# Kernel tuning notes

Hardware: AMD Instinct MI355X
Metric: run time of the kernel (lower is better)

The kernel has to match this reference:

```python
import jax, jax.numpy as jnp
import numpy as np

NUM_HEADS = 12


def get_rel_pos(q_size, k_size, rel_pos):
    # rel_pos: (2*max(q,k)-1, head_dim); sizes match table here so no resize.
    max_rel_dist = int(2 * max(q_size, k_size) - 1)
    if rel_pos.shape[0] != max_rel_dist:
        rel_pos = jax.image.resize(rel_pos, (max_rel_dist, rel_pos.shape[1]), method='linear')
    q_coords = jnp.arange(q_size)[:, None] * max(k_size / q_size, 1.0)
    k_coords = jnp.arange(k_size)[None, :] * max(q_size / k_size, 1.0)
    rel = (q_coords - k_coords + (k_size - 1) * max(q_size / k_size, 1.0)).astype(jnp.int32)
    return rel_pos[rel.reshape(-1)].reshape(q_size, k_size, -1)  # (q, k, head_dim)


def setup_inputs() -> dict:
    key = jax.random.key(0)
    ks = jax.random.split(key, 7)
    B, H, W, C = 8, 32, 32, 768
    head_dim = C // NUM_HEADS
    return {
        'x': jax.random.normal(ks[0], (B, H, W, C), jnp.float32),
        'w_qkv': jax.random.normal(ks[1], (C, 3 * C), jnp.float32) * 0.02,
        'b_qkv': jnp.zeros((3 * C,), jnp.float32),
        'rel_pos_h': jax.random.normal(ks[2], (2 * H - 1, head_dim), jnp.float32) * 0.02,
        'rel_pos_w': jax.random.normal(ks[3], (2 * W - 1, head_dim), jnp.float32) * 0.02,
        'w_proj': jax.random.normal(ks[4], (C, C), jnp.float32) * 0.02,
        'b_proj': jnp.zeros((C,), jnp.float32),
    }


def reference(x, w_qkv, b_qkv, rel_pos_h, rel_pos_w, w_proj, b_proj):
    B, H, W, C = x.shape
    heads = NUM_HEADS
    hd = C // heads
    S = H * W
    qkv = x @ w_qkv + b_qkv                                  # (B,H,W,3C)
    qkv = qkv.reshape(B, S, 3, heads, hd).transpose(2, 0, 3, 1, 4)
    qkv = qkv.reshape(3, B * heads, S, hd)
    q, k, v = qkv[0], qkv[1], qkv[2]
    attn = (q * hd ** -0.5) @ k.transpose(0, 2, 1)           # (B*heads, S, S)
    rh = get_rel_pos(H, H, rel_pos_h)                        # (H,H,hd)
    rw = get_rel_pos(W, W, rel_pos_w)                        # (W,W,hd)
    r_q = q.reshape(B * heads, H, W, hd)
    rel_h = jnp.einsum('bhwc,hkc->bhwk', r_q, rh)
    rel_w = jnp.einsum('bhwc,wkc->bhwk', r_q, rw)
    attn = (attn.reshape(B * heads, H, W, H, W)
            + rel_h[:, :, :, :, None]
            + rel_w[:, :, :, None, :]).reshape(B * heads, S, S)
    attn = jax.nn.softmax(attn, axis=-1)
    out = (attn @ v).reshape(B, heads, H, W, hd).transpose(0, 2, 3, 1, 4).reshape(B, H, W, C)
    return out @ w_proj + b_proj
```

## Files before the change

### kernel.cpp

```cpp
#include <hip/hip_runtime.h>
#include <hip/hip_bf16.h>

#define BATCH 8
#define SEQ   1024
#define CH    768
#define NH    12
#define HD    64
#define BH    96
#define N_QKV 2304

#define LOG2E 1.44269504088896f

typedef __attribute__((ext_vector_type(8))) short bfrag;
typedef __attribute__((ext_vector_type(4))) short short4v;
typedef __attribute__((ext_vector_type(4))) float ffrag;

__device__ __forceinline__ short f2bf(float x) {
    __hip_bfloat16 h = __float2bfloat16(x);
    return *reinterpret_cast<short*>(&h);
}
__device__ __forceinline__ float bf2f(short b) {
    __hip_bfloat16 h;
    *reinterpret_cast<short*>(&h) = b;
    return __bfloat162float(h);
}
__device__ __forceinline__ void split2(float x, short& hi, short& lo) {
    short h = f2bf(x);
    hi = h;
    lo = f2bf(x - bf2f(h));
}
__device__ __forceinline__ void async_copy16(void* lds, const void* g) {
    __builtin_amdgcn_global_load_lds(
        (const __attribute__((address_space(1))) void*)g,
        (__attribute__((address_space(3))) void*)lds, 16, 0, 0);
}

__global__ __launch_bounds__(256) void prep(
    const float* __restrict__ x,
    const float* __restrict__ w_qkv, const float* __restrict__ w_proj,
    short* __restrict__ Xh,
    short* __restrict__ WqhT,
    short* __restrict__ WphT, short* __restrict__ WplT)
{
    __shared__ float ts[32][33];
    const int tid = threadIdx.x;
    const int bid = blockIdx.x;

    if (bid < 512) {
        const int n4 = (BATCH * SEQ * CH) / 4;
        for (int i = bid * 256 + tid; i < n4; i += 512 * 256) {
            float4 f = ((const float4*)x)[i];
            short4v h;
            h[0] = f2bf(f.x); h[1] = f2bf(f.y); h[2] = f2bf(f.z); h[3] = f2bf(f.w);
            ((short4v*)Xh)[i] = h;
        }
        return;
    }
    if (bid < 2240) {
        int t = bid - 512;
        const int bx = t % 72, by = t / 72;
        const int r0 = by * 32, c0 = bx * 32;
        #pragma unroll
        for (int i = 0; i < 4; ++i) {
            int idx = tid + i * 256;
            int rr = idx >> 5, cc = idx & 31;
            ts[rr][cc] = w_qkv[(size_t)(r0 + rr) * N_QKV + c0 + cc];
        }
        __syncthreads();
        #pragma unroll
        for (int i = 0; i < 4; ++i) {
            int idx = tid + i * 256;
            int rr = idx >> 5, cc = idx & 31;
            WqhT[(size_t)(c0 + rr) * CH + r0 + cc] = f2bf(ts[cc][rr]);
        }
        return;
    }
    {
        int t = bid - 2240;
        const int bx = t % 24, by = t / 24;
        const int r0 = by * 32, c0 = bx * 32;
        #pragma unroll
        for (int i = 0; i < 4; ++i) {
            int idx = tid + i * 256;
            int rr = idx >> 5, cc = idx & 31;
            ts[rr][cc] = w_proj[(size_t)(r0 + rr) * CH + c0 + cc];
        }
        __syncthreads();
        #pragma unroll
        for (int i = 0; i < 4; ++i) {
            int idx = tid + i * 256;
            int rr = idx >> 5, cc = idx & 31;
            short h, l;
            split2(ts[cc][rr], h, l);
            WphT[(size_t)(c0 + rr) * CH + r0 + cc] = h;
            WplT[(size_t)(c0 + rr) * CH + r0 + cc] = l;
        }
    }
}

__device__ __forceinline__ void gemm_core1(
    short* lds,
    const short* __restrict__ Ah, const short* __restrict__ BhT,
    int m0, int n0, ffrag acc[4][4])
{
    const int tid = threadIdx.x;
    const int wave = tid >> 6, lane = tid & 63;
    const int quad = lane >> 4, l16 = lane & 15;
    const int wm = (wave & 1) * 64, wn = (wave >> 1) * 64;

    const int arr  = wave >> 1;
    const int half = wave & 1;
    const short* src = arr ? BhT : Ah;
    const int row0 = (arr ? n0 : m0) + half * 64;
    const size_t lane_off = (size_t)(lane >> 3) * CH + (size_t)((lane & 7) ^ (lane >> 3)) * 8;
    const short* sbase = src + (size_t)row0 * CH + lane_off;
    short* ldsw = lds + arr * 8192 + half * 4096;

    for (int c = 0; c < 12; ++c) {
        __syncthreads();
        #pragma unroll
        for (int i = 0; i < 8; ++i)
            async_copy16(ldsw + i * 512, sbase + (size_t)i * 8 * CH + c * 64);
        __syncthreads();

        #pragma unroll
        for (int kc = 0; kc < 2; ++kc) {
            bfrag ah[4], bh[4];
            const int xs = ((kc * 4 + quad) ^ (l16 & 7)) * 8;
            #pragma unroll
            for (int i = 0; i < 4; ++i) {
                ah[i] = *(const bfrag*)&lds[(wm + i * 16 + l16) * 64 + xs];
                bh[i] = *(const bfrag*)&lds[8192 + (wn + i * 16 + l16) * 64 + xs];
            }
            #pragma unroll
            for (int mi = 0; mi < 4; ++mi)
                #pragma unroll
                for (int ni = 0; ni < 4; ++ni)
                    acc[mi][ni] = __builtin_amdgcn_mfma_f32_16x16x32_bf16(ah[mi], bh[ni], acc[mi][ni], 0, 0, 0);
        }
    }
}

__device__ __forceinline__ void gemm_core3(
    short* lds,
    const short* __restrict__ Ah, const short* __restrict__ Al,
    const short* __restrict__ BhT, const short* __restrict__ BlT,
    int m0, int n0, ffrag acc[4][4])
{
    const int tid = threadIdx.x;
    const int wave = tid >> 6, lane = tid & 63;
    const int quad = lane >> 4, l16 = lane & 15;
    const int wm = (wave & 1) * 64, wn = (wave >> 1) * 64;

    const short* src;
    int row0;
    if (wave == 0)      { src = Ah;  row0 = m0; }
    else if (wave == 1) { src = Al;  row0 = m0; }
    else if (wave == 2) { src = BhT; row0 = n0; }
    else                { src = BlT; row0 = n0; }
    const size_t lane_off = (size_t)(lane >> 3) * CH + (size_t)((lane & 7) ^ (lane >> 3)) * 8;
    const short* sbase = src + (size_t)row0 * CH + lane_off;
    short* ldsw = lds + wave * 8192;

    for (int c = 0; c < 12; ++c) {
        __syncthreads();
        #pragma unroll
        for (int i = 0; i < 16; ++i)
            async_copy16(ldsw + i * 512, sbase + (size_t)i * 8 * CH + c * 64);
        __syncthreads();

        #pragma unroll
        for (int kc = 0; kc < 2; ++kc) {
            bfrag ah[4], al[4], bh[4], bl[4];
            const int xs = ((kc * 4 + quad) ^ (l16 & 7)) * 8;
            #pragma unroll
            for (int i = 0; i < 4; ++i) {
                int ra = (wm + i * 16 + l16) * 64 + xs;
                int rb = (wn + i * 16 + l16) * 64 + xs;
                ah[i] = *(const bfrag*)&lds[ra];
                al[i] = *(const bfrag*)&lds[8192 + ra];
                bh[i] = *(const bfrag*)&lds[16384 + rb];
                bl[i] = *(const bfrag*)&lds[24576 + rb];
            }
            #pragma unroll
            for (int mi = 0; mi < 4; ++mi)
                #pragma unroll
                for (int ni = 0; ni < 4; ++ni) {
                    acc[mi][ni] = __builtin_amdgcn_mfma_f32_16x16x32_bf16(ah[mi], bh[ni], acc[mi][ni], 0, 0, 0);
                    acc[mi][ni] = __builtin_amdgcn_mfma_f32_16x16x32_bf16(ah[mi], bl[ni], acc[mi][ni], 0, 0, 0);
                    acc[mi][ni] = __builtin_amdgcn_mfma_f32_16x16x32_bf16(al[mi], bh[ni], acc[mi][ni], 0, 0, 0);
                }
        }
    }
}

__global__ __launch_bounds__(256) void gemm_qkv_mfma(
    const short* __restrict__ Xh,
    const short* __restrict__ WhT,
    const float* __restrict__ bias,
    short* __restrict__ qh, short* __restrict__ kh, short* __restrict__ vT)
{
    __shared__ short lds[2 * 8192];
    const int id  = blockIdx.x;
    const int xcd = id & 7;
    const int per = id >> 3;
    const int m0 = (xcd * 8 + per / 18) * 128;
    const int n0 = (per % 18) * 128;
    const int which = n0 / CH;

    ffrag acc[4][4];
    #pragma unroll
    for (int i = 0; i < 4; ++i)
        #pragma unroll
        for (int j = 0; j < 4; ++j) acc[i][j] = (ffrag){0.f, 0.f, 0.f, 0.f};

    gemm_core1(lds, Xh, WhT, m0, n0, acc);

    const int tid = threadIdx.x;
    const int wave = tid >> 6, lane = tid & 63;
    const int quad = lane >> 4, l16 = lane & 15;
    const int wm = (wave & 1) * 64, wn = (wave >> 1) * 64;
    const int b = m0 >> 10;

    #pragma unroll
    for (int ni = 0; ni < 4; ++ni) {
        int n = n0 + wn + ni * 16 + l16;
        float bv = bias[n];
        int nin = n - which * CH;
        int head = nin >> 6, d = nin & 63;
        #pragma unroll
        for (int mi = 0; mi < 4; ++mi) {
            if (which == 2) {
                int s_base = (m0 & 1023) + wm + mi * 16 + quad * 4;
                short4v pk;
                #pragma unroll
                for (int r = 0; r < 4; ++r) pk[r] = f2bf(acc[mi][ni][r] + bv);
                *(short4v*)&vT[((size_t)(b * NH + head) * HD + d) * SEQ + s_base] = pk;
            } else {
                const float scale = (which == 0) ? 0.125f * LOG2E : 1.0f;
                short* dst = (which == 0) ? qh : kh;
                #pragma unroll
                for (int r = 0; r < 4; ++r) {
                    int m = m0 + wm + mi * 16 + quad * 4 + r;
                    int s = m & 1023;
                    dst[((size_t)(b * NH + head) * SEQ + s) * HD + d] =
                        f2bf((acc[mi][ni][r] + bv) * scale);
                }
            }
        }
    }
}

__global__ __launch_bounds__(256) void gemm_proj_mfma(
    const short* __restrict__ Ah, const short* __restrict__ Al,
    const short* __restrict__ WhT, const short* __restrict__ WlT,
    const float* __restrict__ bias, float* __restrict__ out)
{
    __shared__ short lds[4 * 8192];
    const int id  = blockIdx.x;
    const int xcd = id & 7;
    const int per = id >> 3;
    const int m0 = (xcd * 8 + per / 6) * 128;
    const int n0 = (per % 6) * 128;

    ffrag acc[4][4];
    #pragma unroll
    for (int i = 0; i < 4; ++i)
        #pragma unroll
        for (int j = 0; j < 4; ++j) acc[i][j] = (ffrag){0.f, 0.f, 0.f, 0.f};

    gemm_core3(lds, Ah, Al, WhT, WlT, m0, n0, acc);

    const int tid = threadIdx.x;
    const int wave = tid >> 6, lane = tid & 63;
    const int quad = lane >> 4, l16 = lane & 15;
    const int wm = (wave & 1) * 64, wn = (wave >> 1) * 64;

    #pragma unroll
    for (int ni = 0; ni < 4; ++ni) {
        int n = n0 + wn + ni * 16 + l16;
        float bv = bias[n];
        #pragma unroll
        for (int mi = 0; mi < 4; ++mi)
            #pragma unroll
            for (int r = 0; r < 4; ++r) {
                int m = m0 + wm + mi * 16 + quad * 4 + r;
                out[(size_t)m * CH + n] = acc[mi][ni][r] + bv;
            }
    }
}

__global__ __launch_bounds__(256, 3) void attn_kernel(
    const short* __restrict__ qh,
    const short* __restrict__ kh_g, const short* __restrict__ vT_g,
    const float* __restrict__ rph,
    const float* __restrict__ rpw,
    short* __restrict__ aoh, short* __restrict__ aol)
{
    const int fid   = blockIdx.x;
    const int xcd   = fid & 7;
    const int inner = fid >> 3;
    const int s0    = (inner & 7) * 128;
    const int bh    = xcd * 12 + (inner >> 3);

    const int tid  = threadIdx.x;
    const int wave = tid >> 6;
    const int lane = tid & 63;
    const int quad = lane >> 4;
    const int l16  = lane & 15;

    __shared__ short Kh[64 * 64];
    __shared__ short Vth[64 * 64];
    __shared__ short Th[128][68];
    __shared__ short Tw_Ps[128 * 72];

    bfrag qfh[2][2];
    #pragma unroll
    for (int g = 0; g < 2; ++g) {
        const size_t qrow = ((size_t)bh * SEQ + s0 + wave * 32 + g * 16 + l16) * HD;
        #pragma unroll
        for (int kc = 0; kc < 2; ++kc)
            qfh[g][kc] = *(const bfrag*)(qh + qrow + kc * 32 + quad * 8);
    }

    #pragma unroll
    for (int table = 0; table < 2; ++table) {
        const float* tbl = table ? rpw : rph;
        #pragma unroll
        for (int n0r = 0; n0r < 64; n0r += 16) {
            int r = n0r + l16;
            bfrag bfr[2];
            #pragma unroll
            for (int kc = 0; kc < 2; ++kc) {
                if (r < 63) {
                    const float* trow = tbl + (size_t)r * HD + kc * 32 + quad * 8;
                    float4 f0 = *(const float4*)(trow);
                    float4 f1 = *(const float4*)(trow + 4);
                    float xs[8] = {f0.x, f0.y, f0.z, f0.w, f1.x, f1.y, f1.z, f1.w};
                    #pragma unroll
                    for (int j = 0; j < 8; ++j) bfr[kc][j] = f2bf(xs[j]);
                } else {
                    #pragma unroll
                    for (int j = 0; j < 8; ++j) bfr[kc][j] = 0;
                }
            }
            #pragma unroll
            for (int g = 0; g < 2; ++g) {
                ffrag acc = {0.f, 0.f, 0.f, 0.f};
                acc = __builtin_amdgcn_mfma_f32_16x16x32_bf16(qfh[g][0], bfr[0], acc, 0, 0, 0);
                acc = __builtin_amdgcn_mfma_f32_16x16x32_bf16(qfh[g][1], bfr[1], acc, 0, 0, 0);
                int row = wave * 32 + g * 16 + quad * 4;
                #pragma unroll
                for (int reg = 0; reg < 4; ++reg) {
                    short v = f2bf(acc[reg] * 8.0f);
                    if (table) Tw_Ps[(row + reg) * 72 + n0r + l16] = v;
                    else       Th[row + reg][n0r + l16] = v;
                }
            }
        }
    }

    float tw_r[2][2][4];
    #pragma unroll
    for (int g = 0; g < 2; ++g) {
        int qloc = wave * 32 + g * 16 + l16;
        int wq = g * 16 + l16;
        #pragma unroll
        for (int p = 0; p < 2; ++p)
            #pragma unroll
            for (int reg = 0; reg < 4; ++reg)
                tw_r[g][p][reg] = bf2f(Tw_Ps[qloc * 72 + (wq - (p * 16 + quad * 4 + reg) + 31)]);
    }
    const int hq_w = (s0 >> 5) + wave;

    float l_part[2] = {0.f, 0.f};
    ffrag Ot[2][4];
    #pragma unroll
    for (int g = 0; g < 2; ++g)
        #pragma unroll
        for (int t = 0; t < 4; ++t) Ot[g][t] = (ffrag){0.f, 0.f, 0.f, 0.f};

    const size_t bh_koff = (size_t)bh * SEQ * HD;
    const size_t bh_voff = (size_t)bh * HD * SEQ;
    const size_t klane = (size_t)(lane >> 3) * HD + (size_t)((lane & 7) ^ (lane >> 3)) * 8;
    const size_t vlane = (size_t)(lane >> 3) * SEQ + (size_t)((lane & 7) ^ (lane >> 3)) * 8;

    for (int c = 0; c < 16; ++c) {
        __syncthreads();
        #pragma unroll
        for (int j = 0; j < 2; ++j) {
            int i = wave * 2 + j;
            async_copy16(Kh + i * 512,
                         kh_g + bh_koff + (size_t)(c * 64 + i * 8) * HD + klane);
            async_copy16(Vth + i * 512,
                         vT_g + bh_voff + (size_t)(i * 8) * SEQ + c * 64 + vlane);
        }
        __syncthreads();

        float th_r[2][2];
        #pragma unroll
        for (int g = 0; g < 2; ++g) {
            int qloc = wave * 32 + g * 16 + l16;
            th_r[g][0] = bf2f(Th[qloc][hq_w - 2 * c + 31]);
            th_r[g][1] = bf2f(Th[qloc][hq_w - 2 * c - 1 + 31]);
        }

        #pragma unroll
        for (int kt = 0; kt < 4; ++kt) {
            bfrag kbh[2];
            #pragma unroll
            for (int kc = 0; kc < 2; ++kc) {
                int xs = ((kc * 4 + quad) ^ (l16 & 7)) * 8;
                kbh[kc] = *(const bfrag*)&Kh[(kt * 16 + l16) * 64 + xs];
            }
            const int hp = kt >> 1, wp = kt & 1;
            #pragma unroll
            for (int g = 0; g < 2; ++g) {
                ffrag acc;
                #pragma unroll
                for (int reg = 0; reg < 4; ++reg)
                    acc[reg] = th_r[g][hp] + tw_r[g][wp][reg];
                acc = __builtin_amdgcn_mfma_f32_16x16x32_bf16(kbh[0], qfh[g][0], acc, 0, 0, 0);
                acc = __builtin_amdgcn_mfma_f32_16x16x32_bf16(kbh[1], qfh[g][1], acc, 0, 0, 0);
                short4v pk;
                #pragma unroll
                for (int reg = 0; reg < 4; ++reg) {
                    float p = exp2f(acc[reg]);
                    l_part[g] += p;
                    pk[reg] = f2bf(p);
                }
                *(short4v*)&Tw_Ps[(wave * 32 + g * 16 + l16) * 72 + kt * 16 + quad * 4] = pk;
            }
        }

        bfrag pf[2][2];
        #pragma unroll
        for (int g = 0; g < 2; ++g)
            #pragma unroll
            for (int kc2 = 0; kc2 < 2; ++kc2)
                pf[g][kc2] = *(const bfrag*)&Tw_Ps[(wave * 32 + g * 16 + l16) * 72 + kc2 * 32 + quad * 8];

        #pragma unroll
        for (int t = 0; t < 4; ++t) {
            int d = t * 16 + l16;
            int x0 = ((0 + quad) ^ (l16 & 7)) * 8;
            int x1 = ((4 + quad) ^ (l16 & 7)) * 8;
            bfrag vh0 = *(const bfrag*)&Vth[d * 64 + x0];
            bfrag vh1 = *(const bfrag*)&Vth[d * 64 + x1];
            #pragma unroll
            for (int g = 0; g < 2; ++g) {
                Ot[g][t] = __builtin_amdgcn_mfma_f32_16x16x32_bf16(pf[g][0], vh0, Ot[g][t], 0, 0, 0);
                Ot[g][t] = __builtin_amdgcn_mfma_f32_16x16x32_bf16(pf[g][1], vh1, Ot[g][t], 0, 0, 0);
            }
        }
    }

    {
        int b = bh / NH, head = bh % NH;
        #pragma unroll
        for (int g = 0; g < 2; ++g) {
            float r = l_part[g];
            r += __shfl_xor(r, 16, 64);
            r += __shfl_xor(r, 32, 64);
            float invl = 1.f / r;
            float inv[4];
            #pragma unroll
            for (int reg = 0; reg < 4; ++reg)
                inv[reg] = __shfl(invl, quad * 4 + reg, 16);
            #pragma unroll
            for (int t = 0; t < 4; ++t) {
                #pragma unroll
                for (int reg = 0; reg < 4; ++reg) {
                    int s_ = s0 + wave * 32 + g * 16 + quad * 4 + reg;
                    int d = t * 16 + l16;
                    size_t idx = ((size_t)(b * SEQ + s_)) * CH + head * HD + d;
                    short h, l;
                    split2(Ot[g][t][reg] * inv[reg], h, l);
                    aoh[idx] = h;
                    aol[idx] = l;
                }
            }
        }
    }
}

extern "C" void kernel_launch(void* const* d_in, const int* in_sizes, int n_in,
                              void* d_out, int out_size, void* d_ws, size_t ws_size,
                              hipStream_t stream) {
    const float* x       = (const float*)d_in[0];
    const float* w_qkv   = (const float*)d_in[1];
    const float* b_qkv   = (const float*)d_in[2];
    const float* rph     = (const float*)d_in[3];
    const float* rpw     = (const float*)d_in[4];
    const float* w_proj  = (const float*)d_in[5];
    const float* b_proj  = (const float*)d_in[6];
    float* out = (float*)d_out;

    const size_t NTOK = (size_t)BATCH * SEQ;
    const size_t XSZ  = NTOK * CH;
    const size_t WQSZ = (size_t)N_QKV * CH;
    const size_t WPSZ = (size_t)CH * CH;
    short* Xh   = (short*)d_ws;
    short* AoL  = Xh + XSZ;
    short* WqhT = AoL + XSZ;
    short* WphT = WqhT + WQSZ;
    short* WplT = WphT + WPSZ;
    short* qh = WplT + WPSZ;
    short* kh = qh + XSZ;
    short* vT = kh + XSZ;
    short* aoh = Xh;
    short* aol = AoL;

    prep<<<dim3(2816), 256, 0, stream>>>(x, w_qkv, w_proj,
                                         Xh, WqhT, WphT, WplT);
    gemm_qkv_mfma<<<dim3(1152), 256, 0, stream>>>(Xh, WqhT, b_qkv,
                                                  qh, kh, vT);
    attn_kernel<<<dim3(768), 256, 0, stream>>>(qh, kh, vT,
                                               rph, rpw, aoh, aol);
    gemm_proj_mfma<<<dim3(384), 256, 0, stream>>>(aoh, aol, WphT, WplT,
                                                  b_proj, out);
}
```

Baseline: 231.1 us.

## Prefetch next K/V tile into LDS while computing on register-held fragments

Each iteration now loads all K and V fragments for the current chunk from LDS into registers, syncs, and then issues the async copy of the next chunk into the same single LDS buffer. This overlaps the global-to-LDS transfer with the QK, softmax and PV compute. The P staging buffer is shrunk to a 64-element row stride with an XOR swizzle in place of the padded 72 stride, to avoid bank conflicts. The extra register-held fragments raise VGPR pressure and may lower occupancy.

New measurement: 226.2 us. 2.1% less time.

```diff
diff --git a/kernel.cpp b/kernel.cpp
--- a/kernel.cpp
+++ b/kernel.cpp
@@ -312,7 +312,7 @@
     __shared__ short Kh[64 * 64];
     __shared__ short Vth[64 * 64];
     __shared__ short Th[128][68];
-    __shared__ short Tw_Ps[128 * 72];
+    __shared__ short Tw_Ps[128 * 68];
 
     bfrag qfh[2][2];
     #pragma unroll
@@ -353,7 +353,7 @@
                 #pragma unroll
                 for (int reg = 0; reg < 4; ++reg) {
                     short v = f2bf(acc[reg] * 8.0f);
-                    if (table) Tw_Ps[(row + reg) * 72 + n0r + l16] = v;
+                    if (table) Tw_Ps[(row + reg) * 68 + n0r + l16] = v;
                     else       Th[row + reg][n0r + l16] = v;
                 }
             }
@@ -369,7 +369,7 @@
         for (int p = 0; p < 2; ++p)
             #pragma unroll
             for (int reg = 0; reg < 4; ++reg)
-                tw_r[g][p][reg] = bf2f(Tw_Ps[qloc * 72 + (wq - (p * 16 + quad * 4 + reg) + 31)]);
+                tw_r[g][p][reg] = bf2f(Tw_Ps[qloc * 68 + (wq - (p * 16 + quad * 4 + reg) + 31)]);
     }
     const int hq_w = (s0 >> 5) + wave;
 
@@ -385,17 +385,47 @@
     const size_t klane = (size_t)(lane >> 3) * HD + (size_t)((lane & 7) ^ (lane >> 3)) * 8;
     const size_t vlane = (size_t)(lane >> 3) * SEQ + (size_t)((lane & 7) ^ (lane >> 3)) * 8;
 
+    const int ps_row = (wave * 32 + l16) * 64;
+    const int ps_wsl = ((quad >> 1)) * 8 + (quad & 1) * 4;
+
+    #pragma unroll
+    for (int j = 0; j < 2; ++j) {
+        int i = wave * 2 + j;
+        async_copy16(Kh + i * 512, kh_g + bh_koff + (size_t)(i * 8) * HD + klane);
+        async_copy16(Vth + i * 512, vT_g + bh_voff + (size_t)(i * 8) * SEQ + vlane);
+    }
+    __syncthreads();
+
     for (int c = 0; c < 16; ++c) {
-        __syncthreads();
-        #pragma unroll
-        for (int j = 0; j < 2; ++j) {
-            int i = wave * 2 + j;
-            async_copy16(Kh + i * 512,
-                         kh_g + bh_koff + (size_t)(c * 64 + i * 8) * HD + klane);
-            async_copy16(Vth + i * 512,
-                         vT_g + bh_voff + (size_t)(i * 8) * SEQ + c * 64 + vlane);
-        }
-        __syncthreads();
+        bfrag kf[4][2], vf[4][2];
+        #pragma unroll
+        for (int kt = 0; kt < 4; ++kt)
+            #pragma unroll
+            for (int kc = 0; kc < 2; ++kc) {
+                int xs = ((kc * 4 + quad) ^ (l16 & 7)) * 8;
+                kf[kt][kc] = *(const bfrag*)&Kh[(kt * 16 + l16) * 64 + xs];
+            }
+        #pragma unroll
+        for (int t = 0; t < 4; ++t) {
+            int d = t * 16 + l16;
+            #pragma unroll
+            for (int h = 0; h < 2; ++h) {
+                int xv = ((h * 4 + quad) ^ (l16 & 7)) * 8;
+                vf[t][h] = *(const bfrag*)&Vth[d * 64 + xv];
+            }
+        }
+        __syncthreads();
+
+        if (c < 15) {
+            #pragma unroll
+            for (int j = 0; j < 2; ++j) {
+                int i = wave * 2 + j;
+                async_copy16(Kh + i * 512,
+                             kh_g + bh_koff + (size_t)((c + 1) * 64 + i * 8) * HD + klane);
+                async_copy16(Vth + i * 512,
+                             vT_g + bh_voff + (size_t)(i * 8) * SEQ + (c + 1) * 64 + vlane);
+            }
+        }
 
         float th_r[2][2];
         #pragma unroll
@@ -407,12 +437,6 @@
 
         #pragma unroll
         for (int kt = 0; kt < 4; ++kt) {
-            bfrag kbh[2];
-            #pragma unroll
-            for (int kc = 0; kc < 2; ++kc) {
-                int xs = ((kc * 4 + quad) ^ (l16 & 7)) * 8;
-                kbh[kc] = *(const bfrag*)&Kh[(kt * 16 + l16) * 64 + xs];
-            }
             const int hp = kt >> 1, wp = kt & 1;
             #pragma unroll
             for (int g = 0; g < 2; ++g) {
@@ -420,8 +444,8 @@
                 #pragma unroll
                 for (int reg = 0; reg < 4; ++reg)
                     acc[reg] = th_r[g][hp] + tw_r[g][wp][reg];
-                acc = __builtin_amdgcn_mfma_f32_16x16x32_bf16(kbh[0], qfh[g][0], acc, 0, 0, 0);
-                acc = __builtin_amdgcn_mfma_f32_16x16x32_bf16(kbh[1], qfh[g][1], acc, 0, 0, 0);
+                acc = __builtin_amdgcn_mfma_f32_16x16x32_bf16(kf[kt][0], qfh[g][0], acc, 0, 0, 0);
+                acc = __builtin_amdgcn_mfma_f32_16x16x32_bf16(kf[kt][1], qfh[g][1], acc, 0, 0, 0);
                 short4v pk;
                 #pragma unroll
                 for (int reg = 0; reg < 4; ++reg) {
@@ -429,7 +453,8 @@
                     l_part[g] += p;
                     pk[reg] = f2bf(p);
                 }
-                *(short4v*)&Tw_Ps[(wave * 32 + g * 16 + l16) * 72 + kt * 16 + quad * 4] = pk;
+                int slot = ((kt * 2 + (quad >> 1)) ^ (l16 & 7)) * 8 + (quad & 1) * 4;
+                *(short4v*)&Tw_Ps[ps_row + g * 1024 + slot] = pk;
             }
         }
 
@@ -437,22 +462,20 @@
         #pragma unroll
         for (int g = 0; g < 2; ++g)
             #pragma unroll
-            for (int kc2 = 0; kc2 < 2; ++kc2)
-                pf[g][kc2] = *(const bfrag*)&Tw_Ps[(wave * 32 + g * 16 + l16) * 72 + kc2 * 32 + quad * 8];
-
-        #pragma unroll
-        for (int t = 0; t < 4; ++t) {
-            int d = t * 16 + l16;
-            int x0 = ((0 + quad) ^ (l16 & 7)) * 8;
-            int x1 = ((4 + quad) ^ (l16 & 7)) * 8;
-            bfrag vh0 = *(const bfrag*)&Vth[d * 64 + x0];
-            bfrag vh1 = *(const bfrag*)&Vth[d * 64 + x1];
+            for (int kc2 = 0; kc2 < 2; ++kc2) {
+                int xp = ((kc2 * 4 + quad) ^ (l16 & 7)) * 8;
+                pf[g][kc2] = *(const bfrag*)&Tw_Ps[ps_row + g * 1024 + xp];
+            }
+
+        #pragma unroll
+        for (int t = 0; t < 4; ++t)
             #pragma unroll
             for (int g = 0; g < 2; ++g) {
-                Ot[g][t] = __builtin_amdgcn_mfma_f32_16x16x32_bf16(pf[g][0], vh0, Ot[g][t], 0, 0, 0);
-                Ot[g][t] = __builtin_amdgcn_mfma_f32_16x16x32_bf16(pf[g][1], vh1, Ot[g][t], 0, 0, 0);
-            }
-        }
+                Ot[g][t] = __builtin_amdgcn_mfma_f32_16x16x32_bf16(pf[g][0], vf[t][0], Ot[g][t], 0, 0, 0);
+                Ot[g][t] = __builtin_amdgcn_mfma_f32_16x16x32_bf16(pf[g][1], vf[t][1], Ot[g][t], 0, 0, 0);
+            }
+
+        __syncthreads();
     }
 
     {
```
